# Kernel tuning notes

Hardware: AMD Instinct MI355X
Metric: run time of the kernel (lower is better)

The kernel has to match this reference:

```python
import jax, jax.numpy as jnp
import numpy as np

# Dims from GlobalFractalRouterConfig defaults
B, D, FP, H, NF, A = 65536, 512, 64, 256, 4, 32


def _norm(x):
    # F.normalize(dim=-1) with eps=1e-12
    return x / jnp.clip(jnp.linalg.norm(x, axis=-1, keepdims=True), 1e-12)


def setup_inputs() -> dict:
    key = jax.random.key(0)
    ks = jax.random.split(key, 12)
    s = 0.02
    return {
        "features": jax.random.normal(ks[0], (B, D), jnp.float32),
        "source_fingerprint": jax.random.normal(ks[1], (FP,), jnp.float32),
        "target_fingerprint": jax.random.normal(ks[2], (FP,), jnp.float32),
        # field_generators: NF stacked (Linear(D+FP,H) -> GELU -> Linear(H,1))
        "Wf1": jax.random.normal(ks[3], (NF, D + FP, H), jnp.float32) * s,
        "bf1": jnp.zeros((NF, H), jnp.float32),
        "Wf2": jax.random.normal(ks[4], (NF, H), jnp.float32) * s,
        "bf2": jnp.zeros((NF,), jnp.float32),
        # compat_proj: Linear(2*FP, NF)
        "Wc": jax.random.normal(ks[5], (2 * FP, NF), jnp.float32) * s,
        "bc": jnp.zeros((NF,), jnp.float32),
        # gate_net: Linear(2*NF+FP, H) -> GELU -> Linear(H, D) -> Sigmoid
        "Wg1": jax.random.normal(ks[6], (2 * NF + FP, H), jnp.float32) * s,
        "bg1": jnp.zeros((H,), jnp.float32),
        "Wg2": jax.random.normal(ks[7], (H, D), jnp.float32) * s,
        "bg2": jnp.zeros((D,), jnp.float32),
        # AnchorBank
        "E": jax.random.normal(ks[8], (A, D), jnp.float32) * s,  # anchor_embeddings
        "Wfp": jax.random.normal(ks[9], (D, D), jnp.float32) * s,  # feature_proj
        "bfp": jnp.zeros((D,), jnp.float32),
        "Wfq": jax.random.normal(ks[10], (FP, D), jnp.float32) * s,  # fingerprint_proj
        "bfq": jnp.zeros((D,), jnp.float32),
    }


def _potential(feats, fp_vec, Wf1, bf1, Wf2, bf2):
    # AdjacentGate.compute_potential, all fields vectorized
    b = feats.shape[0]
    comb = jnp.concatenate(
        [feats, jnp.broadcast_to(fp_vec, (b, fp_vec.shape[0]))], axis=-1
    )  # [B, D+FP]
    h = jax.nn.gelu(jnp.einsum('bi,fih->bfh', comb, Wf1) + bf1, approximate=False)
    return jnp.einsum('bfh,fh->bf', h, Wf2) + bf2  # [B, NF]


def reference(features, source_fingerprint, target_fingerprint,
              Wf1, bf1, Wf2, bf2, Wc, bc, Wg1, bg1, Wg2, bg2,
              E, Wfp, bfp, Wfq, bfq):
    b = features.shape[0]
    # --- AdjacentGate ---
    p_src = _potential(features, source_fingerprint, Wf1, bf1, Wf2, bf2)
    p_tgt = _potential(features, target_fingerprint, Wf1, bf1, Wf2, bf2)
    gradient = p_tgt - p_src  # [B, NF]
    fp_comb = jnp.concatenate([source_fingerprint, target_fingerprint])  # [2*FP]
    compat = jnp.tanh(fp_comb @ Wc + bc)  # [NF]
    gate_in = jnp.concatenate(
        [gradient,
         jnp.broadcast_to(compat, (b, compat.shape[0])),
         jnp.broadcast_to(source_fingerprint, (b, source_fingerprint.shape[0]))],
        axis=-1)  # [B, 2*NF+FP]
    gate = jax.nn.sigmoid(
        jax.nn.gelu(gate_in @ Wg1 + bg1, approximate=False) @ Wg2 + bg2)  # [B, D]
    gated = features * gate
    # --- AnchorBank ---
    feat_proj = _norm(gated @ Wfp + bfp)  # [B, D]
    anchors_norm = _norm(E)  # [A, D]
    aff = feat_proj @ anchors_norm.T  # [B, A]
    fp_proj = source_fingerprint @ Wfq + bfq  # [D]
    aff = aff + 0.3 * (anchors_norm @ fp_proj)
    aff = jax.nn.softmax(aff, axis=-1)
    anchor_features = aff @ E  # [B, D]
    return gated + anchor_features
```

## Files before the change

kernel.cpp:

```cpp
#include <hip/hip_runtime.h>
#include <hip/hip_bf16.h>

typedef unsigned short u16;
typedef __attribute__((ext_vector_type(8))) __bf16 bf16x8;
typedef __attribute__((ext_vector_type(8))) short  s16x8;
typedef __attribute__((ext_vector_type(4))) short  s16x4;
typedef __attribute__((ext_vector_type(4))) float  f32x4;

#define NB 65536
#define OFF_GRAD   0u
#define OFF_SUMSQ  1048576u
#define OFF_CONSTS 1310720u
#define OFF_WF1T   1327104u
#define OFF_WG2T   2375680u
#define OFF_WFPT   2637824u
#define OFF_ET     3162112u
#define OFF_AFF    3194880u
#define OFF_GATED  7389184u
#define WS_NEEDED  74498048u
#define CI_SRC   0
#define CI_TGT   1024
#define CI_C0    2048
#define CI_INVE  2304
#define CI_ABIAS 2336

__device__ inline float bf2f(u16 u) { union { unsigned int i; float f; } v; v.i = ((unsigned int)u) << 16; return v.f; }
__device__ inline u16 f2bf(float f) { union { float f; unsigned int i; } v; v.f = f; return (u16)((v.i + 0x7fffu + ((v.i >> 16) & 1u)) >> 16); }
__device__ inline float gelu(float x) {
  float z = 1.5957691216f * x * (1.0f + 0.044715f * x * x);
  return x * __builtin_amdgcn_rcpf(1.0f + __expf(-z));
}
__device__ inline float sigm(float x) { return __builtin_amdgcn_rcpf(1.0f + __expf(-x)); }

typedef __attribute__((address_space(3))) unsigned int as3_u32;
typedef __attribute__((address_space(1))) unsigned int as1_u32;
__device__ __forceinline__ void gload16(const u16* g, u16* l) {
  __builtin_amdgcn_global_load_lds((const as1_u32*)g, (as3_u32*)l, 16, 0, 0);
}

__global__ __launch_bounds__(256) void k_cvt(const float* __restrict__ feat, u16* __restrict__ featbf) {
  int idx = (blockIdx.x << 8) + threadIdx.x;
  const float4* src = (const float4*)feat + (idx << 1);
  float4 v0 = src[0], v1 = src[1];
  s16x8 o;
  o[0] = (short)f2bf(v0.x); o[1] = (short)f2bf(v0.y);
  o[2] = (short)f2bf(v0.z); o[3] = (short)f2bf(v0.w);
  o[4] = (short)f2bf(v1.x); o[5] = (short)f2bf(v1.y);
  o[6] = (short)f2bf(v1.z); o[7] = (short)f2bf(v1.w);
  *(s16x8*)(featbf + (idx << 3)) = o;
}

__global__ __launch_bounds__(256) void k_pre(
    const float* __restrict__ sfp, const float* __restrict__ tfp,
    const float* __restrict__ wf1, const float* __restrict__ bf1,
    const float* __restrict__ wc,  const float* __restrict__ bc,
    const float* __restrict__ wg1, const float* __restrict__ bg1,
    const float* __restrict__ wfq, const float* __restrict__ bfq,
    const float* __restrict__ E,   float* __restrict__ consts)
{
  __shared__ float s_s[64], s_t[64], s_c[4], s_fp[512];
  const int t = threadIdx.x;
  const int b = blockIdx.x;
  if (t < 64) { s_s[t] = sfp[t]; s_t[t] = tfp[t]; }
  __syncthreads();
  if (b < 8) {
    if (t < 128) {
      int n = b * 128 + t;
      int f = n >> 8, h = n & 255;
      float as = bf1[f * 256 + h];
      float at = as;
      const float* col = wf1 + f * 147456 + 512 * 256 + h;
      #pragma unroll 8
      for (int j = 0; j < 64; ++j) {
        float wv = col[j * 256];
        as += s_s[j] * wv; at += s_t[j] * wv;
      }
      consts[CI_SRC + n] = as;
      consts[CI_TGT + n] = at;
    }
  } else if (b == 8) {
    if (t < 4) {
      float a = bc[t];
      for (int j = 0; j < 64; ++j)
        a += s_s[j] * wc[j * 4 + t] + s_t[j] * wc[(64 + j) * 4 + t];
      s_c[t] = tanhf(a);
    }
    __syncthreads();
    float a = bg1[t];
    #pragma unroll
    for (int f = 0; f < 4; ++f) a += s_c[f] * wg1[(4 + f) * 256 + t];
    for (int j = 0; j < 64; ++j) a += s_s[j] * wg1[(8 + j) * 256 + t];
    consts[CI_C0 + t] = a;
  } else {
    for (int d = t; d < 512; d += 256) {
      float a = bfq[d];
      for (int j = 0; j < 64; ++j) a += s_s[j] * wfq[j * 512 + d];
      s_fp[d] = a;
    }
    __syncthreads();
    if (t < 32) {
      float ss = 0.f, dot = 0.f;
      for (int d = 0; d < 512; ++d) {
        float e = E[t * 512 + d];
        ss += e * e; dot += e * s_fp[d];
      }
      float inv = 1.0f / fmaxf(sqrtf(ss), 1e-12f);
      consts[CI_INVE + t] = inv;
      consts[CI_ABIAS + t] = 0.3f * inv * dot;
    }
  }
}

__global__ __launch_bounds__(256) void k_transpose(
    const float* __restrict__ wf1, const float* __restrict__ wg2,
    const float* __restrict__ wfp, const float* __restrict__ E,
    u16* __restrict__ ws16)
{
  int tile = blockIdx.x;
  const float* src; u16* dst; int K, N, tl;
  if (tile < 512)      { int f = tile >> 7; tl = tile & 127; src = wf1 + f * 147456; dst = ws16 + (OFF_WF1T >> 1) + f * 131072; K = 512; N = 256; }
  else if (tile < 640) { tl = tile - 512; src = wg2; dst = ws16 + (OFF_WG2T >> 1); K = 256; N = 512; }
  else if (tile < 896) { tl = tile - 640; src = wfp; dst = ws16 + (OFF_WFPT >> 1); K = 512; N = 512; }
  else                 { tl = tile - 896; src = E;   dst = ws16 + (OFF_ET   >> 1); K = 32;  N = 512; }
  int ntn = N >> 5;
  int r0 = (tl / ntn) << 5, c0 = (tl % ntn) << 5;
  __shared__ float T[32][33];
  const int t = threadIdx.x;
  {
    int r = t >> 3, c4 = (t & 7) << 2;
    float4 v = *(const float4*)(src + (r0 + r) * N + c0 + c4);
    T[r][c4] = v.x; T[r][c4 + 1] = v.y; T[r][c4 + 2] = v.z; T[r][c4 + 3] = v.w;
  }
  __syncthreads();
  {
    int c = t >> 3, r4 = (t & 7) << 2;
    s16x4 v;
    v[0] = (short)f2bf(T[r4 + 0][c]); v[1] = (short)f2bf(T[r4 + 1][c]);
    v[2] = (short)f2bf(T[r4 + 2][c]); v[3] = (short)f2bf(T[r4 + 3][c]);
    *(s16x4*)(dst + (c0 + c) * K + r0 + r4) = v;
  }
}

__global__ __launch_bounds__(256, 2) void k_potential(
    const u16* __restrict__ featbf, const u16* __restrict__ wf1t,
    const float* __restrict__ wf2,  const float* __restrict__ consts,
    float* __restrict__ grad)
{
  __shared__ u16 Al[2][128][32];
  __shared__ u16 Bl[2][256][32];
  const int wg = blockIdx.x;
  const int s  = ((wg & 7) << 8) + (wg >> 3);
  const int f  = s & 3;
  const int col0 = f << 8;
  const int row0 = (s >> 2) << 7;
  const int t = threadIdx.x;
  const int w = t >> 6, lane = t & 63, lr = lane & 15, lq = lane >> 4;
  const int gr  = lane >> 2;
  const int gcs = ((lane & 3) ^ ((lane >> 3) & 3)) << 3;
  const int ca  = (lq ^ ((lr >> 1) & 3)) << 3;

  f32x4 acc[2][16];
  #pragma unroll
  for (int i = 0; i < 2; ++i)
    #pragma unroll
    for (int j = 0; j < 16; ++j) { f32x4 z = {0.f, 0.f, 0.f, 0.f}; acc[i][j] = z; }

#define STAGE_P(buf, k0) { \
    _Pragma("unroll") for (int j = 0; j < 2; ++j) { int rb = (j << 6) + (w << 4); \
      gload16(featbf + (row0 + rb + gr) * 512 + (k0) + gcs, &Al[buf][rb][0]); } \
    _Pragma("unroll") for (int j = 0; j < 4; ++j) { int rb = (j << 6) + (w << 4); \
      gload16(wf1t + (col0 + rb + gr) * 512 + (k0) + gcs, &Bl[buf][rb][0]); } }

#define COMP_P(buf) { bf16x8 a[2]; \
    _Pragma("unroll") for (int rt = 0; rt < 2; ++rt) \
      a[rt] = *(const bf16x8*)&Al[buf][(w << 5) + (rt << 4) + lr][ca]; \
    _Pragma("unroll") for (int ct = 0; ct < 16; ++ct) { \
      bf16x8 bb = *(const bf16x8*)&Bl[buf][(ct << 4) + lr][ca]; \
      acc[0][ct] = __builtin_amdgcn_mfma_f32_16x16x32_bf16(a[0], bb, acc[0][ct], 0, 0, 0); \
      acc[1][ct] = __builtin_amdgcn_mfma_f32_16x16x32_bf16(a[1], bb, acc[1][ct], 0, 0, 0); } }

  STAGE_P(0, 0);
  __syncthreads();
  #pragma unroll
  for (int k0 = 0; k0 < 512; k0 += 64) {
    STAGE_P(1, k0 + 32);
    COMP_P(0);
    __syncthreads();
    if (k0 + 64 < 512) STAGE_P(0, k0 + 64);
    COMP_P(1);
    __syncthreads();
  }
#undef STAGE_P
#undef COMP_P
  float part[2][4] = {{0, 0, 0, 0}, {0, 0, 0, 0}};
  #pragma unroll
  for (int ct = 0; ct < 16; ++ct) {
    int n = col0 + (ct << 4) + lr;
    float so = consts[CI_SRC + n];
    float to = consts[CI_TGT + n];
    float w2 = wf2[n];
    #pragma unroll
    for (int rt = 0; rt < 2; ++rt)
      #pragma unroll
      for (int j = 0; j < 4; ++j) {
        float c = acc[rt][ct][j];
        part[rt][j] += (gelu(c + to) - gelu(c + so)) * w2;
      }
  }
  #pragma unroll
  for (int m = 1; m <= 8; m <<= 1)
    #pragma unroll
    for (int rt = 0; rt < 2; ++rt)
      #pragma unroll
      for (int j = 0; j < 4; ++j)
        part[rt][j] += __shfl_xor(part[rt][j], m, 64);
  if (lr == 0) {
    #pragma unroll
    for (int rt = 0; rt < 2; ++rt)
      #pragma unroll
      for (int j = 0; j < 4; ++j) {
        int r = row0 + (w << 5) + (rt << 4) + (lq << 2) + j;
        grad[r * 4 + f] = part[rt][j];
      }
  }
}

__global__ __launch_bounds__(256, 2) void k_gate(
    const u16* __restrict__ featbf, const float* __restrict__ grad,
    const float* __restrict__ wg1,  const u16* __restrict__ wg2t,
    const float* __restrict__ bg2,  const float* __restrict__ consts,
    u16* __restrict__ gated)
{
  __shared__ u16 Hl[32768];
  __shared__ u16 Bl[2][128][32];
  const int wg = blockIdx.x;
  const int s  = ((wg & 7) << 8) + (wg >> 3);
  const int col0 = (s & 3) << 7;
  const int row0 = (s >> 2) << 7;
  const int t = threadIdx.x;
  const int w = t >> 6, lane = t & 63, lr = lane & 15, lq = lane >> 4;
  const int gr  = lane >> 2;
  const int gcs = ((lane & 3) ^ ((lane >> 3) & 3)) << 3;
  const int ca  = (lq ^ ((lr >> 1) & 3)) << 3;

#define STAGE_G(buf, k0) { \
    _Pragma("unroll") for (int j = 0; j < 2; ++j) { int rb = (j << 6) + (w << 4); \
      gload16(wg2t + (col0 + rb + gr) * 256 + (k0) + gcs, &Bl[buf][rb][0]); } }

  STAGE_G(0, 0);

  {
    float wv[4], c0v = consts[CI_C0 + t];
    const int tc = t >> 3, tw = t & 7;
    #pragma unroll
    for (int f = 0; f < 4; ++f) wv[f] = wg1[f * 256 + t];
    for (int i = 0; i < 128; ++i) {
      float4 g = *(const float4*)(grad + ((row0 + i) << 2));
      float p = c0v + g.x * wv[0] + g.y * wv[1] + g.z * wv[2] + g.w * wv[3];
      Hl[i * 256 + ((tc ^ ((i >> 1) & 7)) << 3) + tw] = f2bf(gelu(p));
    }
  }
  f32x4 acc[2][8];
  #pragma unroll
  for (int i = 0; i < 2; ++i)
    #pragma unroll
    for (int j = 0; j < 8; ++j) { f32x4 z = {0.f, 0.f, 0.f, 0.f}; acc[i][j] = z; }

#define COMP_G(buf, k0) { bf16x8 a[2]; \
    _Pragma("unroll") for (int rt = 0; rt < 2; ++rt) { \
      int r = (w << 5) + (rt << 4) + lr; \
      int cq = (((k0) >> 3) + lq) ^ (lr >> 1); \
      a[rt] = *(const bf16x8*)&Hl[r * 256 + (cq << 3)]; } \
    _Pragma("unroll") for (int ct = 0; ct < 8; ++ct) { \
      bf16x8 bb = *(const bf16x8*)&Bl[buf][(ct << 4) + lr][ca]; \
      acc[0][ct] = __builtin_amdgcn_mfma_f32_16x16x32_bf16(a[0], bb, acc[0][ct], 0, 0, 0); \
      acc[1][ct] = __builtin_amdgcn_mfma_f32_16x16x32_bf16(a[1], bb, acc[1][ct], 0, 0, 0); } }

  __syncthreads();
  #pragma unroll
  for (int k0 = 0; k0 < 256; k0 += 64) {
    STAGE_G(1, k0 + 32);
    COMP_G(0, k0);
    __syncthreads();
    if (k0 + 64 < 256) STAGE_G(0, k0 + 64);
    COMP_G(1, k0 + 32);
    __syncthreads();
  }
#undef STAGE_G
#undef COMP_G
  u16* Gl = Hl;
  #pragma unroll
  for (int ct = 0; ct < 8; ++ct) {
    int n = col0 + (ct << 4) + lr;
    float bv = bg2[n];
    #pragma unroll
    for (int rt = 0; rt < 2; ++rt)
      #pragma unroll
      for (int j = 0; j < 4; ++j) {
        int r = (w << 5) + (rt << 4) + (lq << 2) + j;
        Gl[r * 136 + (ct << 4) + lr] = f2bf(sigm(acc[rt][ct][j] + bv));
      }
  }
  __syncthreads();
  #pragma unroll
  for (int it = 0; it < 8; ++it) {
    int s2 = (it << 8) + t;
    int r = s2 >> 4, c8 = (s2 & 15) << 3;
    s16x8 f8 = *(const s16x8*)(featbf + (row0 + r) * 512 + col0 + c8);
    s16x8 g8 = *(const s16x8*)(Gl + r * 136 + c8);
    s16x8 o;
    #pragma unroll
    for (int j = 0; j < 8; ++j)
      o[j] = (short)f2bf(bf2f((u16)f8[j]) * bf2f((u16)g8[j]));
    *(s16x8*)(gated + (row0 + r) * 512 + col0 + c8) = o;
  }
}

__global__ __launch_bounds__(256, 2) void k_proj(
    const u16* __restrict__ gated, const u16* __restrict__ wfpt,
    const float* __restrict__ bfp, u16* __restrict__ y,
    float* __restrict__ sumsq)
{
  __shared__ u16 U[33792];
  u16* A0 = U;
  u16* B0 = U + 4096;
  u16* A1 = U + 12288;
  u16* B1 = U + 16384;
  const int wg = blockIdx.x;
  const int s  = ((wg & 7) << 7) + (wg >> 3);
  const int col0 = (s & 1) << 8;
  const int row0 = (s >> 1) << 7;
  const int t = threadIdx.x;
  const int w = t >> 6, lane = t & 63, lr = lane & 15, lq = lane >> 4;
  const int gr  = lane >> 2;
  const int gcs = ((lane & 3) ^ ((lane >> 3) & 3)) << 3;
  const int ca  = (lq ^ ((lr >> 1) & 3)) << 3;

  f32x4 acc[2][16];
  #pragma unroll
  for (int i = 0; i < 2; ++i)
    #pragma unroll
    for (int j = 0; j < 16; ++j) { f32x4 z = {0.f, 0.f, 0.f, 0.f}; acc[i][j] = z; }

#define STAGE_J(Ab, Bb, k0) { \
    _Pragma("unroll") for (int j = 0; j < 2; ++j) { int rb = (j << 6) + (w << 4); \
      gload16(gated + (row0 + rb + gr) * 512 + (k0) + gcs, Ab + rb * 32); } \
    _Pragma("unroll") for (int j = 0; j < 4; ++j) { int rb = (j << 6) + (w << 4); \
      gload16(wfpt + (col0 + rb + gr) * 512 + (k0) + gcs, Bb + rb * 32); } }

#define COMP_J(Ab, Bb) { bf16x8 a[2]; \
    _Pragma("unroll") for (int rt = 0; rt < 2; ++rt) \
      a[rt] = *(const bf16x8*)&Ab[((w << 5) + (rt << 4) + lr) * 32 + ca]; \
    _Pragma("unroll") for (int ct = 0; ct < 16; ++ct) { \
      bf16x8 bb = *(const bf16x8*)&Bb[((ct << 4) + lr) * 32 + ca]; \
      acc[0][ct] = __builtin_amdgcn_mfma_f32_16x16x32_bf16(a[0], bb, acc[0][ct], 0, 0, 0); \
      acc[1][ct] = __builtin_amdgcn_mfma_f32_16x16x32_bf16(a[1], bb, acc[1][ct], 0, 0, 0); } }

  STAGE_J(A0, B0, 0);
  __syncthreads();
  #pragma unroll
  for (int k0 = 0; k0 < 512; k0 += 64) {
    STAGE_J(A1, B1, k0 + 32);
    COMP_J(A0, B0);
    __syncthreads();
    if (k0 + 64 < 512) STAGE_J(A0, B0, k0 + 64);
    COMP_J(A1, B1);
    __syncthreads();
  }
#undef STAGE_J
#undef COMP_J
  float part[2][4] = {{0, 0, 0, 0}, {0, 0, 0, 0}};
  #pragma unroll
  for (int ct = 0; ct < 16; ++ct) {
    float bv = bfp[col0 + (ct << 4) + lr];
    #pragma unroll
    for (int rt = 0; rt < 2; ++rt)
      #pragma unroll
      for (int j = 0; j < 4; ++j) {
        acc[rt][ct][j] += bv;
        part[rt][j] += acc[rt][ct][j] * acc[rt][ct][j];
      }
  }
  #pragma unroll
  for (int m = 1; m <= 8; m <<= 1)
    #pragma unroll
    for (int rt = 0; rt < 2; ++rt)
      #pragma unroll
      for (int j = 0; j < 4; ++j)
        part[rt][j] += __shfl_xor(part[rt][j], m, 64);
  if (lr == 0) {
    #pragma unroll
    for (int rt = 0; rt < 2; ++rt)
      #pragma unroll
      for (int j = 0; j < 4; ++j)
        atomicAdd(&sumsq[row0 + (w << 5) + (rt << 4) + (lq << 2) + j], part[rt][j]);
  }
  u16* Yl = U;
  #pragma unroll
  for (int ct = 0; ct < 16; ++ct)
    #pragma unroll
    for (int rt = 0; rt < 2; ++rt)
      #pragma unroll
      for (int j = 0; j < 4; ++j) {
        int r = (w << 5) + (rt << 4) + (lq << 2) + j;
        Yl[r * 264 + (ct << 4) + lr] = f2bf(acc[rt][ct][j]);
      }
  __syncthreads();
  #pragma unroll
  for (int it = 0; it < 16; ++it) {
    int s2 = (it << 8) + t;
    int r = s2 >> 5, c8 = (s2 & 31) << 3;
    *(s16x8*)(y + (row0 + r) * 512 + col0 + c8) = *(const s16x8*)(Yl + r * 264 + c8);
  }
}

__global__ __launch_bounds__(256, 2) void k_aff(
    const u16* __restrict__ y, const float* __restrict__ E,
    const float* __restrict__ sumsq, const float* __restrict__ consts,
    u16* __restrict__ aff)
{
  __shared__ u16 El[32][520];
  __shared__ u16 Aa[2][256][32];
  const int row0 = blockIdx.x << 8;
  const int t = threadIdx.x;
  const int w = t >> 6, lane = t & 63, lr = lane & 15, lq = lane >> 4;
  const int gr  = lane >> 2;
  const int gcs = ((lane & 3) ^ ((lane >> 3) & 3)) << 3;
  const int ca  = (lq ^ ((lr >> 1) & 3)) << 3;

#define STAGE_A(buf, k0) { \
    _Pragma("unroll") for (int j = 0; j < 4; ++j) { int rb = (j << 6) + (w << 4); \
      gload16(y + (row0 + rb + gr) * 512 + (k0) + gcs, &Aa[buf][rb][0]); } }

  STAGE_A(0, 0);
  #pragma unroll
  for (int i = 0; i < 16; ++i) {
    int s = (i << 8) + t;
    int a = s >> 7, c4 = (s & 127) << 2;
    float4 v = *(const float4*)(E + a * 512 + c4);
    s16x4 b;
    b[0] = (short)f2bf(v.x); b[1] = (short)f2bf(v.y);
    b[2] = (short)f2bf(v.z); b[3] = (short)f2bf(v.w);
    *(s16x4*)&El[a][c4] = b;
  }
  f32x4 acc[4][2];
  #pragma unroll
  for (int i = 0; i < 4; ++i)
    #pragma unroll
    for (int j = 0; j < 2; ++j) { f32x4 z = {0.f, 0.f, 0.f, 0.f}; acc[i][j] = z; }

#define COMP_A(buf, k0) { \
    bf16x8 b0 = *(const bf16x8*)&El[lr][(k0) + (lq << 3)]; \
    bf16x8 b1 = *(const bf16x8*)&El[16 + lr][(k0) + (lq << 3)]; \
    _Pragma("unroll") for (int rt = 0; rt < 4; ++rt) { \
      bf16x8 a = *(const bf16x8*)&Aa[buf][(w << 6) + (rt << 4) + lr][ca]; \
      acc[rt][0] = __builtin_amdgcn_mfma_f32_16x16x32_bf16(a, b0, acc[rt][0], 0, 0, 0); \
      acc[rt][1] = __builtin_amdgcn_mfma_f32_16x16x32_bf16(a, b1, acc[rt][1], 0, 0, 0); } }

  __syncthreads();
  #pragma unroll
  for (int k0 = 0; k0 < 512; k0 += 64) {
    STAGE_A(1, k0 + 32);
    COMP_A(0, k0);
    __syncthreads();
    if (k0 + 64 < 512) STAGE_A(0, k0 + 64);
    COMP_A(1, k0 + 32);
    __syncthreads();
  }
#undef STAGE_A
#undef COMP_A
  float iv0 = consts[CI_INVE + lr],  iv1 = consts[CI_INVE + 16 + lr];
  float ab0 = consts[CI_ABIAS + lr], ab1 = consts[CI_ABIAS + 16 + lr];
  #pragma unroll
  for (int rt = 0; rt < 4; ++rt) {
    #pragma unroll
    for (int j = 0; j < 4; ++j) {
      int r = row0 + (w << 6) + (rt << 4) + (lq << 2) + j;
      float invn = 1.0f / fmaxf(sqrtf(sumsq[r]), 1e-12f);
      float v0 = acc[rt][0][j] * iv0 * invn + ab0;
      float v1 = acc[rt][1][j] * iv1 * invn + ab1;
      float mx = fmaxf(v0, v1);
      #pragma unroll
      for (int m = 1; m <= 8; m <<= 1) mx = fmaxf(mx, __shfl_xor(mx, m, 64));
      float e0 = __expf(v0 - mx), e1 = __expf(v1 - mx);
      float sm = e0 + e1;
      #pragma unroll
      for (int m = 1; m <= 8; m <<= 1) sm += __shfl_xor(sm, m, 64);
      float rs = 1.0f / sm;
      aff[r * 32 + lr]      = f2bf(e0 * rs);
      aff[r * 32 + 16 + lr] = f2bf(e1 * rs);
    }
  }
}

__global__ __launch_bounds__(256, 2) void k_out(
    const u16* __restrict__ gated, const u16* __restrict__ aff,
    const u16* __restrict__ et, float* __restrict__ out)
{
  __shared__ u16 ETl[512][40];
  __shared__ u16 Afl[64][40];
  __shared__ u16 Ol[64][520];
  const int row0 = blockIdx.x << 6;
  const int t = threadIdx.x;
  const int w = t >> 6, lane = t & 63, lr = lane & 15, lq = lane >> 4;
  {
    int r = t >> 2, k8 = (t & 3) << 3;
    *(bf16x8*)&Afl[r][k8] = *(const bf16x8*)(aff + (row0 + r) * 32 + k8);
  }
  #pragma unroll
  for (int i = 0; i < 8; ++i) {
    int s = (i << 8) + t;
    int d = s >> 2, k8 = (s & 3) << 3;
    *(bf16x8*)&ETl[d][k8] = *(const bf16x8*)(et + d * 32 + k8);
  }
  __syncthreads();
  bf16x8 a[4];
  #pragma unroll
  for (int rt = 0; rt < 4; ++rt)
    a[rt] = *(const bf16x8*)&Afl[(rt << 4) + lr][lq << 3];
  f32x4 z = {0.f, 0.f, 0.f, 0.f};
  #pragma unroll
  for (int ct = 0; ct < 8; ++ct) {
    bf16x8 bb = *(const bf16x8*)&ETl[(w << 7) + (ct << 4) + lr][lq << 3];
    #pragma unroll
    for (int rt = 0; rt < 4; ++rt) {
      f32x4 o = __builtin_amdgcn_mfma_f32_16x16x32_bf16(a[rt], bb, z, 0, 0, 0);
      #pragma unroll
      for (int j = 0; j < 4; ++j)
        Ol[(rt << 4) + (lq << 2) + j][(w << 7) + (ct << 4) + lr] = f2bf(o[j]);
    }
  }
  __syncthreads();
  #pragma unroll
  for (int it = 0; it < 32; ++it) {
    int s = (it << 8) + t;
    int r = s >> 7, c4 = (s & 127) << 2;
    s16x4 g4 = *(const s16x4*)(gated + (row0 + r) * 512 + c4);
    s16x4 a4 = *(const s16x4*)(&Ol[0][0] + r * 520 + c4);
    float4 o;
    o.x = bf2f((u16)g4[0]) + bf2f((u16)a4[0]);
    o.y = bf2f((u16)g4[1]) + bf2f((u16)a4[1]);
    o.z = bf2f((u16)g4[2]) + bf2f((u16)a4[2]);
    o.w = bf2f((u16)g4[3]) + bf2f((u16)a4[3]);
    *(float4*)(out + (row0 + r) * 512 + c4) = o;
  }
}

extern "C" void kernel_launch(void* const* d_in, const int* in_sizes, int n_in,
                              void* d_out, int out_size, void* d_ws, size_t ws_size,
                              hipStream_t stream) {
  (void)in_sizes; (void)n_in; (void)out_size;
  if (ws_size < WS_NEEDED) return;
  const float* feat = (const float*)d_in[0];
  const float* sfp  = (const float*)d_in[1];
  const float* tfp  = (const float*)d_in[2];
  const float* wf1  = (const float*)d_in[3];
  const float* bf1  = (const float*)d_in[4];
  const float* wf2  = (const float*)d_in[5];
  const float* wc   = (const float*)d_in[7];
  const float* bc   = (const float*)d_in[8];
  const float* wg1  = (const float*)d_in[9];
  const float* bg1  = (const float*)d_in[10];
  const float* wg2  = (const float*)d_in[11];
  const float* bg2  = (const float*)d_in[12];
  const float* E    = (const float*)d_in[13];
  const float* wfp  = (const float*)d_in[14];
  const float* bfp  = (const float*)d_in[15];
  const float* wfq  = (const float*)d_in[16];
  const float* bfq  = (const float*)d_in[17];

  char* ws = (char*)d_ws;
  float* grad   = (float*)(ws + OFF_GRAD);
  float* sumsq  = (float*)(ws + OFF_SUMSQ);
  float* consts = (float*)(ws + OFF_CONSTS);
  u16* ws16  = (u16*)ws;
  u16* wf1t  = (u16*)(ws + OFF_WF1T);
  u16* wg2t  = (u16*)(ws + OFF_WG2T);
  u16* wfpt  = (u16*)(ws + OFF_WFPT);
  u16* et    = (u16*)(ws + OFF_ET);
  u16* aff   = (u16*)(ws + OFF_AFF);
  u16* gated = (u16*)(ws + OFF_GATED);
  u16* yscr  = (u16*)d_out;
  u16* featbf = (u16*)d_out + 33554432;
  float* out = (float*)d_out;

  hipMemsetAsync(ws + OFF_SUMSQ, 0, 262144, stream);
  k_cvt<<<dim3(16384), dim3(256), 0, stream>>>(feat, featbf);
  k_pre<<<dim3(10), dim3(256), 0, stream>>>(sfp, tfp, wf1, bf1, wc, bc, wg1, bg1, wfq, bfq, E, consts);
  k_transpose<<<dim3(912), dim3(256), 0, stream>>>(wf1, wg2, wfp, E, ws16);
  k_potential<<<dim3(2048), dim3(256), 0, stream>>>(featbf, wf1t, wf2, consts, grad);
  k_gate<<<dim3(2048), dim3(256), 0, stream>>>(featbf, grad, wg1, wg2t, bg2, consts, gated);
  k_proj<<<dim3(1024), dim3(256), 0, stream>>>(gated, wfpt, bfp, yscr, sumsq);
  k_aff<<<dim3(256), dim3(256), 0, stream>>>(yscr, E, sumsq, consts, aff);
  k_out<<<dim3(1024), dim3(256), 0, stream>>>(gated, aff, et, out);
}
```

Before: 635.8 us.

## Fuse anchor affinity GEMM into projection kernel and triple-buffer GEMM pipelines

The projection kernel now multiplies its output tile by E in its epilogue and accumulates partial anchor affinities into a float buffer with atomics. This avoids writing the full bf16 projected matrix and re-reading it in a separate affinity kernel. A small softmax kernel then normalizes the affinities. Separately, the potential and projection GEMM main loops move to a three-stage LDS ring using explicit vmcnt waits, which lets more loads stay in flight. The cost is an extra memset, more atomics, and larger shared memory per block.

```diff
diff --git a/kernel.cpp b/kernel.cpp
--- a/kernel.cpp
+++ b/kernel.cpp
@@ -146,8 +146,7 @@
     const float* __restrict__ wf2,  const float* __restrict__ consts,
     float* __restrict__ grad)
 {
-  __shared__ u16 Al[2][128][32];
-  __shared__ u16 Bl[2][256][32];
+  __shared__ u16 U[36864];
   const int wg = blockIdx.x;
   const int s  = ((wg & 7) << 8) + (wg >> 3);
   const int f  = s & 3;
@@ -165,30 +164,28 @@
     #pragma unroll
     for (int j = 0; j < 16; ++j) { f32x4 z = {0.f, 0.f, 0.f, 0.f}; acc[i][j] = z; }
 
-#define STAGE_P(buf, k0) { \
+#define STAGE_P(bi, k0) { u16* bas = U + (bi) * 12288; \
     _Pragma("unroll") for (int j = 0; j < 2; ++j) { int rb = (j << 6) + (w << 4); \
-      gload16(featbf + (row0 + rb + gr) * 512 + (k0) + gcs, &Al[buf][rb][0]); } \
+      gload16(featbf + (row0 + rb + gr) * 512 + (k0) + gcs, bas + rb * 32); } \
     _Pragma("unroll") for (int j = 0; j < 4; ++j) { int rb = (j << 6) + (w << 4); \
-      gload16(wf1t + (col0 + rb + gr) * 512 + (k0) + gcs, &Bl[buf][rb][0]); } }
-
-#define COMP_P(buf) { bf16x8 a[2]; \
+      gload16(wf1t + (col0 + rb + gr) * 512 + (k0) + gcs, bas + 4096 + rb * 32); } }
+
+#define COMP_P(bi) { const u16* bas = U + (bi) * 12288; bf16x8 a[2]; \
     _Pragma("unroll") for (int rt = 0; rt < 2; ++rt) \
-      a[rt] = *(const bf16x8*)&Al[buf][(w << 5) + (rt << 4) + lr][ca]; \
+      a[rt] = *(const bf16x8*)&bas[((w << 5) + (rt << 4) + lr) * 32 + ca]; \
     _Pragma("unroll") for (int ct = 0; ct < 16; ++ct) { \
-      bf16x8 bb = *(const bf16x8*)&Bl[buf][(ct << 4) + lr][ca]; \
+      bf16x8 bb = *(const bf16x8*)&bas[4096 + ((ct << 4) + lr) * 32 + ca]; \
       acc[0][ct] = __builtin_amdgcn_mfma_f32_16x16x32_bf16(a[0], bb, acc[0][ct], 0, 0, 0); \
       acc[1][ct] = __builtin_amdgcn_mfma_f32_16x16x32_bf16(a[1], bb, acc[1][ct], 0, 0, 0); } }
 
   STAGE_P(0, 0);
-  __syncthreads();
-  #pragma unroll
-  for (int k0 = 0; k0 < 512; k0 += 64) {
-    STAGE_P(1, k0 + 32);
-    COMP_P(0);
-    __syncthreads();
-    if (k0 + 64 < 512) STAGE_P(0, k0 + 64);
-    COMP_P(1);
-    __syncthreads();
+  STAGE_P(1, 32);
+  #pragma unroll
+  for (int tt = 0; tt < 16; ++tt) {
+    if (tt < 15) asm volatile("s_waitcnt vmcnt(6)\n\ts_barrier" ::: "memory");
+    else         asm volatile("s_waitcnt vmcnt(0)\n\ts_barrier" ::: "memory");
+    if (tt < 14) STAGE_P((tt + 2) % 3, (tt + 2) * 32);
+    COMP_P(tt % 3);
   }
 #undef STAGE_P
 #undef COMP_P
@@ -318,14 +315,10 @@
 
 __global__ __launch_bounds__(256, 2) void k_proj(
     const u16* __restrict__ gated, const u16* __restrict__ wfpt,
-    const float* __restrict__ bfp, u16* __restrict__ y,
-    float* __restrict__ sumsq)
-{
-  __shared__ u16 U[33792];
-  u16* A0 = U;
-  u16* B0 = U + 4096;
-  u16* A1 = U + 12288;
-  u16* B1 = U + 16384;
+    const float* __restrict__ bfp, const float* __restrict__ E,
+    float* __restrict__ aff32, float* __restrict__ sumsq)
+{
+  __shared__ u16 U[36864];
   const int wg = blockIdx.x;
   const int s  = ((wg & 7) << 7) + (wg >> 3);
   const int col0 = (s & 1) << 8;
@@ -342,30 +335,28 @@
     #pragma unroll
     for (int j = 0; j < 16; ++j) { f32x4 z = {0.f, 0.f, 0.f, 0.f}; acc[i][j] = z; }
 
-#define STAGE_J(Ab, Bb, k0) { \
+#define STAGE_J(bi, k0) { u16* bas = U + (bi) * 12288; \
     _Pragma("unroll") for (int j = 0; j < 2; ++j) { int rb = (j << 6) + (w << 4); \
-      gload16(gated + (row0 + rb + gr) * 512 + (k0) + gcs, Ab + rb * 32); } \
+      gload16(gated + (row0 + rb + gr) * 512 + (k0) + gcs, bas + rb * 32); } \
     _Pragma("unroll") for (int j = 0; j < 4; ++j) { int rb = (j << 6) + (w << 4); \
-      gload16(wfpt + (col0 + rb + gr) * 512 + (k0) + gcs, Bb + rb * 32); } }
-
-#define COMP_J(Ab, Bb) { bf16x8 a[2]; \
+      gload16(wfpt + (col0 + rb + gr) * 512 + (k0) + gcs, bas + 4096 + rb * 32); } }
+
+#define COMP_J(bi) { const u16* bas = U + (bi) * 12288; bf16x8 a[2]; \
     _Pragma("unroll") for (int rt = 0; rt < 2; ++rt) \
-      a[rt] = *(const bf16x8*)&Ab[((w << 5) + (rt << 4) + lr) * 32 + ca]; \
+      a[rt] = *(const bf16x8*)&bas[((w << 5) + (rt << 4) + lr) * 32 + ca]; \
     _Pragma("unroll") for (int ct = 0; ct < 16; ++ct) { \
-      bf16x8 bb = *(const bf16x8*)&Bb[((ct << 4) + lr) * 32 + ca]; \
+      bf16x8 bb = *(const bf16x8*)&bas[4096 + ((ct << 4) + lr) * 32 + ca]; \
       acc[0][ct] = __builtin_amdgcn_mfma_f32_16x16x32_bf16(a[0], bb, acc[0][ct], 0, 0, 0); \
       acc[1][ct] = __builtin_amdgcn_mfma_f32_16x16x32_bf16(a[1], bb, acc[1][ct], 0, 0, 0); } }
 
-  STAGE_J(A0, B0, 0);
-  __syncthreads();
-  #pragma unroll
-  for (int k0 = 0; k0 < 512; k0 += 64) {
-    STAGE_J(A1, B1, k0 + 32);
-    COMP_J(A0, B0);
-    __syncthreads();
-    if (k0 + 64 < 512) STAGE_J(A0, B0, k0 + 64);
-    COMP_J(A1, B1);
-    __syncthreads();
+  STAGE_J(0, 0);
+  STAGE_J(1, 32);
+  #pragma unroll
+  for (int tt = 0; tt < 16; ++tt) {
+    if (tt < 15) asm volatile("s_waitcnt vmcnt(6)\n\ts_barrier" ::: "memory");
+    else         asm volatile("s_waitcnt vmcnt(0)\n\ts_barrier" ::: "memory");
+    if (tt < 14) STAGE_J((tt + 2) % 3, (tt + 2) * 32);
+    COMP_J(tt % 3);
   }
 #undef STAGE_J
 #undef COMP_J
@@ -395,101 +386,83 @@
       for (int j = 0; j < 4; ++j)
         atomicAdd(&sumsq[row0 + (w << 5) + (rt << 4) + (lq << 2) + j], part[rt][j]);
   }
-  u16* Yl = U;
-  #pragma unroll
-  for (int ct = 0; ct < 16; ++ct)
-    #pragma unroll
-    for (int rt = 0; rt < 2; ++rt)
+  __syncthreads();
+  {
+    int a = t >> 3, cb = (t & 7) << 5;
+    const float* ep = E + a * 512 + col0 + cb;
+    u16* dp = U + 17408 + a * 264 + cb;
+    #pragma unroll
+    for (int i = 0; i < 8; ++i) {
+      float4 v = *(const float4*)(ep + (i << 2));
+      s16x4 b;
+      b[0] = (short)f2bf(v.x); b[1] = (short)f2bf(v.y);
+      b[2] = (short)f2bf(v.z); b[3] = (short)f2bf(v.w);
+      *(s16x4*)(dp + (i << 2)) = b;
+    }
+  }
+  f32x4 acc2[2][2];
+  #pragma unroll
+  for (int i = 0; i < 2; ++i)
+    #pragma unroll
+    for (int j = 0; j < 2; ++j) { f32x4 z = {0.f, 0.f, 0.f, 0.f}; acc2[i][j] = z; }
+  #pragma unroll
+  for (int half = 0; half < 2; ++half) {
+    if (half) __syncthreads();
+    #pragma unroll
+    for (int ct = 0; ct < 8; ++ct)
+      #pragma unroll
+      for (int rt = 0; rt < 2; ++rt)
+        #pragma unroll
+        for (int j = 0; j < 4; ++j) {
+          int r = (w << 5) + (rt << 4) + (lq << 2) + j;
+          U[r * 136 + (ct << 4) + lr] = f2bf(acc[rt][(half << 3) + ct][j]);
+        }
+    __syncthreads();
+    #pragma unroll
+    for (int ks = 0; ks < 4; ++ks) {
+      bf16x8 a0 = *(const bf16x8*)&U[((w << 5) + lr) * 136 + (ks << 5) + (lq << 3)];
+      bf16x8 a1 = *(const bf16x8*)&U[((w << 5) + 16 + lr) * 136 + (ks << 5) + (lq << 3)];
+      bf16x8 b0 = *(const bf16x8*)&U[17408 + lr * 264 + (half << 7) + (ks << 5) + (lq << 3)];
+      bf16x8 b1 = *(const bf16x8*)&U[17408 + (16 + lr) * 264 + (half << 7) + (ks << 5) + (lq << 3)];
+      acc2[0][0] = __builtin_amdgcn_mfma_f32_16x16x32_bf16(a0, b0, acc2[0][0], 0, 0, 0);
+      acc2[0][1] = __builtin_amdgcn_mfma_f32_16x16x32_bf16(a0, b1, acc2[0][1], 0, 0, 0);
+      acc2[1][0] = __builtin_amdgcn_mfma_f32_16x16x32_bf16(a1, b0, acc2[1][0], 0, 0, 0);
+      acc2[1][1] = __builtin_amdgcn_mfma_f32_16x16x32_bf16(a1, b1, acc2[1][1], 0, 0, 0);
+    }
+  }
+  #pragma unroll
+  for (int rt = 0; rt < 2; ++rt)
+    #pragma unroll
+    for (int c2 = 0; c2 < 2; ++c2)
       #pragma unroll
       for (int j = 0; j < 4; ++j) {
-        int r = (w << 5) + (rt << 4) + (lq << 2) + j;
-        Yl[r * 264 + (ct << 4) + lr] = f2bf(acc[rt][ct][j]);
-      }
-  __syncthreads();
-  #pragma unroll
-  for (int it = 0; it < 16; ++it) {
-    int s2 = (it << 8) + t;
-    int r = s2 >> 5, c8 = (s2 & 31) << 3;
-    *(s16x8*)(y + (row0 + r) * 512 + col0 + c8) = *(const s16x8*)(Yl + r * 264 + c8);
-  }
-}
-
-__global__ __launch_bounds__(256, 2) void k_aff(
-    const u16* __restrict__ y, const float* __restrict__ E,
-    const float* __restrict__ sumsq, const float* __restrict__ consts,
-    u16* __restrict__ aff)
-{
-  __shared__ u16 El[32][520];
-  __shared__ u16 Aa[2][256][32];
-  const int row0 = blockIdx.x << 8;
-  const int t = threadIdx.x;
-  const int w = t >> 6, lane = t & 63, lr = lane & 15, lq = lane >> 4;
-  const int gr  = lane >> 2;
-  const int gcs = ((lane & 3) ^ ((lane >> 3) & 3)) << 3;
-  const int ca  = (lq ^ ((lr >> 1) & 3)) << 3;
-
-#define STAGE_A(buf, k0) { \
-    _Pragma("unroll") for (int j = 0; j < 4; ++j) { int rb = (j << 6) + (w << 4); \
-      gload16(y + (row0 + rb + gr) * 512 + (k0) + gcs, &Aa[buf][rb][0]); } }
-
-  STAGE_A(0, 0);
-  #pragma unroll
-  for (int i = 0; i < 16; ++i) {
-    int s = (i << 8) + t;
-    int a = s >> 7, c4 = (s & 127) << 2;
-    float4 v = *(const float4*)(E + a * 512 + c4);
-    s16x4 b;
-    b[0] = (short)f2bf(v.x); b[1] = (short)f2bf(v.y);
-    b[2] = (short)f2bf(v.z); b[3] = (short)f2bf(v.w);
-    *(s16x4*)&El[a][c4] = b;
-  }
-  f32x4 acc[4][2];
-  #pragma unroll
-  for (int i = 0; i < 4; ++i)
-    #pragma unroll
-    for (int j = 0; j < 2; ++j) { f32x4 z = {0.f, 0.f, 0.f, 0.f}; acc[i][j] = z; }
-
-#define COMP_A(buf, k0) { \
-    bf16x8 b0 = *(const bf16x8*)&El[lr][(k0) + (lq << 3)]; \
-    bf16x8 b1 = *(const bf16x8*)&El[16 + lr][(k0) + (lq << 3)]; \
-    _Pragma("unroll") for (int rt = 0; rt < 4; ++rt) { \
-      bf16x8 a = *(const bf16x8*)&Aa[buf][(w << 6) + (rt << 4) + lr][ca]; \
-      acc[rt][0] = __builtin_amdgcn_mfma_f32_16x16x32_bf16(a, b0, acc[rt][0], 0, 0, 0); \
-      acc[rt][1] = __builtin_amdgcn_mfma_f32_16x16x32_bf16(a, b1, acc[rt][1], 0, 0, 0); } }
-
-  __syncthreads();
-  #pragma unroll
-  for (int k0 = 0; k0 < 512; k0 += 64) {
-    STAGE_A(1, k0 + 32);
-    COMP_A(0, k0);
-    __syncthreads();
-    if (k0 + 64 < 512) STAGE_A(0, k0 + 64);
-    COMP_A(1, k0 + 32);
-    __syncthreads();
-  }
-#undef STAGE_A
-#undef COMP_A
-  float iv0 = consts[CI_INVE + lr],  iv1 = consts[CI_INVE + 16 + lr];
-  float ab0 = consts[CI_ABIAS + lr], ab1 = consts[CI_ABIAS + 16 + lr];
-  #pragma unroll
-  for (int rt = 0; rt < 4; ++rt) {
-    #pragma unroll
-    for (int j = 0; j < 4; ++j) {
-      int r = row0 + (w << 6) + (rt << 4) + (lq << 2) + j;
-      float invn = 1.0f / fmaxf(sqrtf(sumsq[r]), 1e-12f);
-      float v0 = acc[rt][0][j] * iv0 * invn + ab0;
-      float v1 = acc[rt][1][j] * iv1 * invn + ab1;
-      float mx = fmaxf(v0, v1);
-      #pragma unroll
-      for (int m = 1; m <= 8; m <<= 1) mx = fmaxf(mx, __shfl_xor(mx, m, 64));
-      float e0 = __expf(v0 - mx), e1 = __expf(v1 - mx);
-      float sm = e0 + e1;
-      #pragma unroll
-      for (int m = 1; m <= 8; m <<= 1) sm += __shfl_xor(sm, m, 64);
-      float rs = 1.0f / sm;
-      aff[r * 32 + lr]      = f2bf(e0 * rs);
-      aff[r * 32 + 16 + lr] = f2bf(e1 * rs);
-    }
+        int r = row0 + (w << 5) + (rt << 4) + (lq << 2) + j;
+        int a = (c2 << 4) + lr;
+        atomicAdd(&aff32[(r << 5) + a], acc2[rt][c2][j]);
+      }
+}
+
+__global__ __launch_bounds__(256) void k_softmax(
+    const float* __restrict__ aff32, const float* __restrict__ sumsq,
+    const float* __restrict__ consts, u16* __restrict__ aff)
+{
+  const int t = threadIdx.x;
+  const int lane = t & 63, wv = t >> 6;
+  const int a = lane & 31, rh = lane >> 5;
+  float ive = consts[CI_INVE + a], ab = consts[CI_ABIAS + a];
+  #pragma unroll
+  for (int it = 0; it < 4; ++it) {
+    int r = (blockIdx.x << 5) + (wv << 3) + (it << 1) + rh;
+    float invy = 1.0f / fmaxf(sqrtf(sumsq[r]), 1e-12f);
+    float v = aff32[(r << 5) + a] * ive * invy + ab;
+    float mx = v;
+    #pragma unroll
+    for (int m = 1; m <= 16; m <<= 1) mx = fmaxf(mx, __shfl_xor(mx, m, 64));
+    float e = __expf(v - mx);
+    float sm = e;
+    #pragma unroll
+    for (int m = 1; m <= 16; m <<= 1) sm += __shfl_xor(sm, m, 64);
+    aff[(r << 5) + a] = f2bf(e * (1.0f / sm));
   }
 }
 
@@ -580,17 +553,18 @@
   u16* et    = (u16*)(ws + OFF_ET);
   u16* aff   = (u16*)(ws + OFF_AFF);
   u16* gated = (u16*)(ws + OFF_GATED);
-  u16* yscr  = (u16*)d_out;
-  u16* featbf = (u16*)d_out + 33554432;
+  float* aff32 = (float*)d_out;
+  u16* featbf  = (u16*)d_out + 33554432;
   float* out = (float*)d_out;
 
   hipMemsetAsync(ws + OFF_SUMSQ, 0, 262144, stream);
+  hipMemsetAsync(d_out, 0, 8388608, stream);
   k_cvt<<<dim3(16384), dim3(256), 0, stream>>>(feat, featbf);
   k_pre<<<dim3(10), dim3(256), 0, stream>>>(sfp, tfp, wf1, bf1, wc, bc, wg1, bg1, wfq, bfq, E, consts);
   k_transpose<<<dim3(912), dim3(256), 0, stream>>>(wf1, wg2, wfp, E, ws16);
   k_potential<<<dim3(2048), dim3(256), 0, stream>>>(featbf, wf1t, wf2, consts, grad);
   k_gate<<<dim3(2048), dim3(256), 0, stream>>>(featbf, grad, wg1, wg2t, bg2, consts, gated);
-  k_proj<<<dim3(1024), dim3(256), 0, stream>>>(gated, wfpt, bfp, yscr, sumsq);
-  k_aff<<<dim3(256), dim3(256), 0, stream>>>(yscr, E, sumsq, consts, aff);
+  k_proj<<<dim3(1024), dim3(256), 0, stream>>>(gated, wfpt, bfp, E, aff32, sumsq);
+  k_softmax<<<dim3(2048), dim3(256), 0, stream>>>(aff32, sumsq, consts, aff);
   k_out<<<dim3(1024), dim3(256), 0, stream>>>(gated, aff, et, out);
 }
```

After: 608.2 us. 1.05x faster.
